# Performance work log

Measured on AMD Instinct MI355X. Metric: run time of the kernel, lower is better.

Reference implementation:

```python
import jax, jax.numpy as jnp
import numpy as np

H = 512; EMB = 300; TAGE = 20; TRE = 20
VOCAB = 50000; NTAGS = 50; NTRANS = 100; NCONST = 80
B = 128; S = 256; T = 512; R = S // 2


def _lstm_scan(x, Wih, Whh, b):
    # x: [N, L, D] -> hidden states [N, L, H]; torch gate order i, f, g, o
    N = x.shape[0]; Hh = Whh.shape[1]
    xg = jnp.einsum('nld,gd->nlg', x, Wih) + b  # precompute input projections
    def step(carry, xg_t):
        h, c = carry
        g = xg_t + h @ Whh.T
        i, f, gg, o = jnp.split(g, 4, axis=-1)
        c = jax.nn.sigmoid(f) * c + jax.nn.sigmoid(i) * jnp.tanh(gg)
        h = jax.nn.sigmoid(o) * jnp.tanh(c)
        return (h, c), h
    h0 = jnp.zeros((N, Hh), x.dtype)
    _, hs = jax.lax.scan(step, (h0, h0), jnp.swapaxes(xg, 0, 1))
    return jnp.swapaxes(hs, 0, 1)


def setup_inputs() -> dict:
    key = jax.random.key(0)
    ks = iter(jax.random.split(key, 40))
    def p(shape, scale):
        return jax.random.normal(next(ks), shape, jnp.float32) * jnp.float32(scale)
    def lstm_p(din):
        s = 1.0 / np.sqrt(H)
        return p((4 * H, din), s), p((4 * H, H), s), p((4 * H,), s)
    inp = {}
    inp['word_idx'] = jax.random.randint(next(ks), (B, S), 0, VOCAB)
    inp['tag_idx'] = jax.random.randint(next(ks), (B, S), 0, NTAGS)
    inp['transition_idx'] = jax.random.randint(next(ks), (B, T), 0, NTRANS)
    inp['label_idx'] = jax.random.randint(next(ks), (B, R), 0, NCONST)
    inp['emb'] = p((VOCAB, EMB), 1.0)
    inp['tag_emb'] = p((NTAGS, TAGE), 1.0)
    inp['tr_emb'] = p((NTRANS, TRE), 1.0)
    inp['const_emb'] = p((NCONST, H), 1.0)
    inp['word_Wih'], inp['word_Whh'], inp['word_b'] = lstm_p(EMB + TAGE)
    inp['tr_Wih'], inp['tr_Whh'], inp['tr_b'] = lstm_p(TRE)
    inp['con_Wih'], inp['con_Whh'], inp['con_b'] = lstm_p(H)
    inp['fwd_Wih'], inp['fwd_Whh'], inp['fwd_b'] = lstm_p(H)
    inp['bwd_Wih'], inp['bwd_Whh'], inp['bwd_b'] = lstm_p(H)
    inp['w2c_W'] = p((H, H), 1.0 / np.sqrt(H)); inp['w2c_b'] = jnp.zeros((H,), jnp.float32)
    inp['red_W'] = p((H, 2 * H), 1.0 / np.sqrt(2 * H)); inp['red_b'] = jnp.zeros((H,), jnp.float32)
    inp['out_W'] = p((NTRANS, 3 * H), 1.0 / np.sqrt(3 * H)); inp['out_b'] = jnp.zeros((NTRANS,), jnp.float32)
    return inp


def reference(word_idx, tag_idx, transition_idx, label_idx, emb, tag_emb, tr_emb, const_emb, word_Wih, word_Whh, word_b, tr_Wih, tr_Whh, tr_b, con_Wih, con_Whh, con_b, fwd_Wih, fwd_Whh, fwd_b, bwd_Wih, bwd_Whh, bwd_b, w2c_W, w2c_b, red_W, red_b, out_W, out_b):
    Bn, Sn = word_idx.shape
    Rn = label_idx.shape[1]
    # initial_word_queue: word emb + tag emb -> word LSTM
    word_in = jnp.concatenate([emb[word_idx], tag_emb[tag_idx]], axis=-1)  # [B,S,EMB+TAGE]
    word_h = _lstm_scan(word_in, word_Wih, word_Whh, word_b)              # [B,S,H]
    # transform_word_to_constituent
    c0 = word_h @ w2c_W.T + w2c_b                                         # [B,S,H]
    # build_constituent: label emb + 2 children through fwd/bwd reduce LSTMs
    lab = const_emb[label_idx]                                            # [B,R,H]
    ch0 = c0[:, 0::2][:, :Rn]; ch1 = c0[:, 1::2][:, :Rn]
    fwd_seq = jnp.stack([lab, ch0, ch1], axis=2).reshape(Bn * Rn, 3, -1)
    bwd_seq = jnp.stack([lab, ch1, ch0], axis=2).reshape(Bn * Rn, 3, -1)
    fh = _lstm_scan(fwd_seq, fwd_Wih, fwd_Whh, fwd_b)[:, -1]
    bh = _lstm_scan(bwd_seq, bwd_Wih, bwd_Whh, bwd_b)[:, -1]
    red = jnp.tanh(jnp.concatenate([fh, bh], -1) @ red_W.T + red_b).reshape(Bn, Rn, -1)
    # push_constituent: constituent LSTMCell scan over built constituents
    const_h = _lstm_scan(red, con_Wih, con_Whh, con_b)[:, -1]             # [B,H]
    # push_transition: transition LSTMCell scan
    tr_h = _lstm_scan(tr_emb[transition_idx], tr_Wih, tr_Whh, tr_b)[:, -1]  # [B,H]
    # forward(): W over concat(word_hx, transition_hx, constituent_hx)
    hx = jnp.concatenate([word_h[:, -1], tr_h, const_h], axis=-1)         # [B,3H]
    return hx @ out_W.T + out_b                                           # [B,NTRANS]
```

## Files before the change

### kernel.cpp

```cpp
#include <hip/hip_runtime.h>

typedef unsigned short u16;
typedef unsigned int u32;
typedef unsigned long long u64;
typedef __attribute__((ext_vector_type(8))) short short8;
typedef __attribute__((ext_vector_type(4))) float f32x4;

namespace {
constexpr int kS  = 256;
constexpr int kT  = 512;
constexpr int kNT = 100;
constexpr int LDST = 40;
}

__device__ __forceinline__ float bf(u16 v){ return __uint_as_float(((u32)v)<<16); }
__device__ __forceinline__ u16 f2bf(float f){
  u32 u = __float_as_uint(f);
  return (u16)((u + 0x7fffu + ((u>>16)&1u)) >> 16);
}
__device__ __forceinline__ float sigm(float x){ return 1.f/(1.f+__expf(-x)); }
__device__ __forceinline__ float tanha(float x){ return 2.f/(1.f+__expf(-2.f*x)) - 1.f; }
__device__ __forceinline__ float wred(float v){
  #pragma unroll
  for (int off=32; off>0; off>>=1) v += __shfl_xor(v, off, 64);
  return v;
}

__device__ __forceinline__ void st_sys_u32(void* p, u32 v){
  __hip_atomic_store((u32*)p, v, __ATOMIC_RELAXED, __HIP_MEMORY_SCOPE_SYSTEM);
}
__device__ __forceinline__ u32 ld_sys_u32(const void* p){
  return __hip_atomic_load((const u32*)p, __ATOMIC_RELAXED, __HIP_MEMORY_SCOPE_SYSTEM);
}

__global__ void k_zero(u32* p, int n){
  const int i = blockIdx.x*256 + threadIdx.x;
  if (i < n) p[i] = 0;
}

struct SeqJob {
  u16* hseq;
  const u16* xg; const int* idx;
  float* c_io;
  const u16* Bw;
  u32* flags;
  int s_begin, s_end, mode, c_store;
};

__global__ __launch_bounds__(256,1) void k_seq2(SeqJob jA, SeqJob jB)
{
  __shared__ u16 Bs[32*520];
  __shared__ float c_lds[128*9];
  __shared__ float sc[4*4*16*20];
  const SeqJob j = (blockIdx.x < 64) ? jA : jB;
  const int gb = blockIdx.x & 63;
  const int tid = threadIdx.x;
  const int ln = tid & 63, w = tid >> 6, wm = w * 32;
  const int fr = ln & 15, koff = (ln >> 4) * 8;
  const int n0 = gb * 32, jh0 = gb * 8;

  for (int e = tid; e < 2048; e += 256) {
    const int cl = e >> 6, kb = (e & 63) * 8;
    *(uint4*)&Bs[cl*520 + kb] = *(const uint4*)&j.Bw[(size_t)(n0+cl)*512 + kb];
  }
  for (int e = tid; e < 1024; e += 256) {
    const int m = e >> 3, jj = e & 7;
    c_lds[m*9 + jj] = j.c_io[(size_t)m*512 + jh0 + jj];
  }
  __syncthreads();

  const size_t aoff0 = (size_t)(wm + fr)*512 + koff;
  const size_t aoff1 = (size_t)(wm + 16 + fr)*512 + koff;
  const int cr = (ln>>4)*4, cc = ln&15;
  const int trow = ln>>2, pp = ln&3, ntp = pp>>1, cp = pp&1;
  const f32x4 z4 = {0.f,0.f,0.f,0.f};

  for (int s = j.s_begin; s < j.s_end; ++s) {
    const u16* Ab = j.hseq + (size_t)((s-1)&255)*65536;
    u16* hout     = j.hseq + (size_t)(s&255)*65536;
    const u16* xgs = (j.mode == 0) ? (j.xg + (size_t)s*262144) : j.xg;

    int xrow[2];
    #pragma unroll
    for (int mt = 0; mt < 2; ++mt) {
      const int m = wm + mt*16 + trow;
      if (j.mode == 1)      xrow[mt] = j.idx[(size_t)m*512 + s];
      else if (j.mode == 0) xrow[mt] = m;
      else                  xrow[mt] = m*128 + s;
    }

    uint4 aq0[16], aq1[16];
    #pragma unroll
    for (int kt = 0; kt < 16; ++kt) {
      aq0[kt] = *(const uint4*)&Ab[aoff0 + kt*32];
      aq1[kt] = *(const uint4*)&Ab[aoff1 + kt*32];
    }
    uint4 xqv[2];
    #pragma unroll
    for (int mt = 0; mt < 2; ++mt)
      xqv[mt] = *(const uint4*)&xgs[(size_t)xrow[mt]*2048 + n0 + ntp*16 + cp*8];

    f32x4 acc[2][2] = {{z4,z4},{z4,z4}};
    #pragma unroll
    for (int kt = 0; kt < 16; ++kt) {
      union { uint4 q; short8 v; } ua, ub;
      ua.q = aq0[kt]; ub.q = aq1[kt];
      const short8 b0 = *(const short8*)&Bs[fr*520 + kt*32 + koff];
      const short8 b1 = *(const short8*)&Bs[(16+fr)*520 + kt*32 + koff];
      acc[0][0] = __builtin_amdgcn_mfma_f32_16x16x32_bf16(ua.v, b0, acc[0][0], 0,0,0);
      acc[0][1] = __builtin_amdgcn_mfma_f32_16x16x32_bf16(ua.v, b1, acc[0][1], 0,0,0);
      acc[1][0] = __builtin_amdgcn_mfma_f32_16x16x32_bf16(ub.v, b0, acc[1][0], 0,0,0);
      acc[1][1] = __builtin_amdgcn_mfma_f32_16x16x32_bf16(ub.v, b1, acc[1][1], 0,0,0);
    }

    #pragma unroll
    for (int mt=0; mt<2; ++mt)
      #pragma unroll
      for (int nt=0; nt<2; ++nt) {
        float* scb = &sc[(size_t)(w*4 + mt*2 + nt)*320];
        #pragma unroll
        for (int ri=0; ri<4; ++ri) scb[(cr+ri)*20 + cc] = acc[mt][nt][ri];
      }
    #pragma unroll
    for (int mt=0; mt<2; ++mt) {
      const int m = wm + mt*16 + trow;
      const float* scb = &sc[(size_t)(w*4+mt*2+ntp)*320 + trow*20 + cp*8];
      const float4 zlo = *(const float4*)&scb[0];
      const float4 zhi = *(const float4*)&scb[4];
      union { uint4 u4; u16 h[8]; } xq;
      xq.u4 = xqv[mt];
      const int cj = m*9 + ntp*4 + cp*2;
      float h0, h1;
      {
        const float i_ = sigm(zlo.x + bf(xq.h[0]));
        const float f_ = sigm(zlo.y + bf(xq.h[1]));
        const float g_ = tanha(zlo.z + bf(xq.h[2]));
        const float o_ = sigm(zlo.w + bf(xq.h[3]));
        const float cn = f_*c_lds[cj] + i_*g_;
        c_lds[cj] = cn;
        h0 = o_*tanha(cn);
      }
      {
        const float i_ = sigm(zhi.x + bf(xq.h[4]));
        const float f_ = sigm(zhi.y + bf(xq.h[5]));
        const float g_ = tanha(zhi.z + bf(xq.h[6]));
        const float o_ = sigm(zhi.w + bf(xq.h[7]));
        const float cn = f_*c_lds[cj+1] + i_*g_;
        c_lds[cj+1] = cn;
        h1 = o_*tanha(cn);
      }
      const u32 pk = (u32)f2bf(h0) | ((u32)f2bf(h1) << 16);
      st_sys_u32(&hout[(size_t)m*512 + jh0 + ntp*4 + cp*2], pk);
    }

    __builtin_amdgcn_s_waitcnt(0);
    __syncthreads();
    if (tid == 0)
      st_sys_u32(j.flags + gb, (u32)s);
    if (s + 1 < j.s_end) {
      if (tid < 64) {
        while (true) {
          u32 f = ld_sys_u32(j.flags + tid);
          if (__all((int)(f >= (u32)s))) break;
          __builtin_amdgcn_s_sleep(1);
        }
      }
      __syncthreads();
    }
  }
  if (j.c_store) {
    __syncthreads();
    for (int e = tid; e < 1024; e += 256) {
      const int m = e >> 3, jj = e & 7;
      j.c_io[(size_t)m*512 + jh0 + jj] = c_lds[m*9 + jj];
    }
  }
}

__device__ __forceinline__ void gemm_core(
    const u16* __restrict__ A, const u16* __restrict__ B, int K,
    int m0, int n0, u16* As, u16* Bs, f32x4 acc[4][4], int tid)
{
  const int lane = tid & 63;
  const int w = tid >> 6;
  const int wm = (w & 1) * 64, wn = (w >> 1) * 64;
  const int fr = lane & 15;
  const int fq = (lane >> 4) * 8;
  for (int k0 = 0; k0 < K; k0 += 32) {
    __syncthreads();
    #pragma unroll
    for (int it = 0; it < 2; ++it) {
      const int l = tid + it * 256;
      const int r = l >> 2, kq = (l & 3) * 8;
      *(uint4*)&As[r * LDST + kq] = *(const uint4*)&A[(size_t)(m0 + r) * K + k0 + kq];
      *(uint4*)&Bs[r * LDST + kq] = *(const uint4*)&B[(size_t)(n0 + r) * K + k0 + kq];
    }
    __syncthreads();
    short8 af[4], bfr[4];
    #pragma unroll
    for (int t = 0; t < 4; ++t) {
      af[t]  = *(const short8*)&As[(wm + t * 16 + fr) * LDST + fq];
      bfr[t] = *(const short8*)&Bs[(wn + t * 16 + fr) * LDST + fq];
    }
    #pragma unroll
    for (int mt = 0; mt < 4; ++mt)
      #pragma unroll
      for (int nt = 0; nt < 4; ++nt)
        acc[mt][nt] = __builtin_amdgcn_mfma_f32_16x16x32_bf16(af[mt], bfr[nt], acc[mt][nt], 0, 0, 0);
  }
}

__global__ __launch_bounds__(256) void k_gemm(
    const u16* __restrict__ A, const u16* __restrict__ B, u16* __restrict__ C,
    const float* __restrict__ bias, int K, int N, int tanh_flag)
{
  __shared__ u16 As[128 * LDST];
  __shared__ u16 Bs[128 * LDST];
  const int tid = threadIdx.x;
  const int m0 = blockIdx.x * 128, n0 = blockIdx.y * 128;
  f32x4 acc[4][4];
  const f32x4 z4 = {0.f, 0.f, 0.f, 0.f};
  #pragma unroll
  for (int mt = 0; mt < 4; ++mt)
    #pragma unroll
    for (int nt = 0; nt < 4; ++nt) acc[mt][nt] = z4;

  gemm_core(A, B, K, m0, n0, As, Bs, acc, tid);

  const int lane = tid & 63;
  const int w = tid >> 6;
  const int wm = (w & 1) * 64, wn = (w >> 1) * 64;
  const int cr = (lane >> 4) * 4, cc = lane & 15;
  #pragma unroll
  for (int mt = 0; mt < 4; ++mt)
    #pragma unroll
    for (int nt = 0; nt < 4; ++nt)
      #pragma unroll
      for (int ri = 0; ri < 4; ++ri) {
        const int row = m0 + wm + mt * 16 + cr + ri;
        const int col = n0 + wn + nt * 16 + cc;
        float v = acc[mt][nt][ri];
        if (bias) v += bias[col];
        if (tanh_flag) v = tanha(v);
        C[(size_t)row * N + col] = f2bf(v);
      }
}

__global__ __launch_bounds__(256) void k_lstm_cat(
    const u16* __restrict__ H, const u16* __restrict__ X,
    const u16* __restrict__ B, const float* __restrict__ bias,
    const int* __restrict__ idx, int cmode, int p0, int first,
    float* __restrict__ c_st, u16* __restrict__ h_out, int h_stride, int h_coloff)
{
  __shared__ u16 As[128 * LDST];
  __shared__ u16 Bs[128 * LDST];
  __shared__ float zb[64 * 128];
  const int tid = threadIdx.x;
  const int m0 = blockIdx.x * 128, n0 = blockIdx.y * 128;
  const int lane = tid & 63;
  const int w = tid >> 6;
  const int wm = (w & 1) * 64, wn = (w >> 1) * 64;
  const int fr = lane & 15, fq = (lane >> 4) * 8;
  f32x4 acc[4][4];
  const f32x4 z4 = {0.f, 0.f, 0.f, 0.f};
  #pragma unroll
  for (int mt = 0; mt < 4; ++mt)
    #pragma unroll
    for (int nt = 0; nt < 4; ++nt) acc[mt][nt] = z4;

  for (int k0 = first ? 512 : 0; k0 < 1024; k0 += 32) {
    __syncthreads();
    #pragma unroll
    for (int it = 0; it < 2; ++it) {
      const int l = tid + it * 256;
      const int r = l >> 2, kq = (l & 3) * 8;
      const int m = m0 + r;
      const u16* src;
      if (k0 < 512) {
        src = H + (size_t)m * 512 + k0 + kq;
      } else {
        long xr;
        if (cmode == 1)      xr = (long)(2 * (m & 127) + p0) * 128 + (m >> 7);
        else if (cmode == 2) xr = (long)idx[m];
        else                 xr = (long)m * 128 + p0;
        src = X + (size_t)xr * 512 + (k0 - 512) + kq;
      }
      *(uint4*)&As[r * LDST + kq] = *(const uint4*)src;
      *(uint4*)&Bs[r * LDST + kq] = *(const uint4*)&B[(size_t)(n0 + r) * 1024 + k0 + kq];
    }
    __syncthreads();
    short8 af[4], bfr[4];
    #pragma unroll
    for (int t = 0; t < 4; ++t) {
      af[t]  = *(const short8*)&As[(wm + t * 16 + fr) * LDST + fq];
      bfr[t] = *(const short8*)&Bs[(wn + t * 16 + fr) * LDST + fq];
    }
    #pragma unroll
    for (int mt = 0; mt < 4; ++mt)
      #pragma unroll
      for (int nt = 0; nt < 4; ++nt)
        acc[mt][nt] = __builtin_amdgcn_mfma_f32_16x16x32_bf16(af[mt], bfr[nt], acc[mt][nt], 0, 0, 0);
  }

  const int cr = (lane >> 4) * 4, cc = lane & 15;
  #pragma unroll
  for (int half = 0; half < 2; ++half) {
    __syncthreads();
    if (wm == half * 64) {
      #pragma unroll
      for (int mt = 0; mt < 4; ++mt)
        #pragma unroll
        for (int nt = 0; nt < 4; ++nt)
          #pragma unroll
          for (int ri = 0; ri < 4; ++ri)
            zb[(mt * 16 + cr + ri) * 128 + wn + nt * 16 + cc] = acc[mt][nt][ri];
    }
    __syncthreads();
    for (int c = tid; c < 2048; c += 256) {
      const int rl = c >> 5;
      const int q  = c & 31;
      const int m  = m0 + half * 64 + rl;
      const int jh = (n0 >> 2) + q;
      const float4 bv = *(const float4*)&bias[n0 + q * 4];
      const float4 zv = *(const float4*)&zb[rl * 128 + q * 4];
      const float i_ = sigm(zv.x + bv.x);
      const float f_ = sigm(zv.y + bv.y);
      const float g_ = tanha(zv.z + bv.z);
      const float o_ = sigm(zv.w + bv.w);
      const size_t ci = (size_t)m * 512 + jh;
      const float cold = first ? 0.f : c_st[ci];
      const float cn = f_ * cold + i_ * g_;
      c_st[ci] = cn;
      h_out[(size_t)m * h_stride + h_coloff + jh] = f2bf(o_ * tanha(cn));
    }
  }
}

__global__ __launch_bounds__(256) void k_gate0(
    const u16* __restrict__ xg, int xg_mode, int p0,
    const int* __restrict__ idx, int istride,
    float* __restrict__ c_st, u16* __restrict__ h_out, int h_stride, int h_coloff, int M)
{
  const int id = blockIdx.x * 256 + threadIdx.x;
  if (id >= M * 512) return;
  const int m = id >> 9, jh = id & 511;
  long xr;
  if (xg_mode == 0) xr = (long)m * p0;
  else              xr = (long)idx[(size_t)m * istride];
  const ushort4 xq = *(const ushort4*)&xg[(size_t)xr * 2048 + jh * 4];
  const float i_ = sigm(bf(xq.x));
  const float g_ = tanha(bf(xq.z));
  const float o_ = sigm(bf(xq.w));
  const float cn = i_ * g_;
  c_st[(size_t)m * 512 + jh] = cn;
  h_out[(size_t)m * h_stride + h_coloff + jh] = f2bf(o_ * tanha(cn));
}

__global__ void k_perm_w(const float* __restrict__ in, u16* __restrict__ out,
                         int Ksrc, int Kfill, int Ktot, int coff)
{
  const int rp = blockIdx.x;
  const int g = rp & 3, jh = rp >> 2;
  const float* src = in + (size_t)(g * 512 + jh) * Ksrc;
  for (int k = threadIdx.x; k < Kfill; k += 256)
    out[(size_t)rp * Ktot + coff + k] = f2bf(k < Ksrc ? src[k] : 0.f);
}
__global__ void k_perm_b(const float* __restrict__ in, float* __restrict__ out)
{
  const int rp = blockIdx.x * 256 + threadIdx.x;
  out[rp] = in[(rp & 3) * 512 + (rp >> 2)];
}
__global__ void k_cvt(const float* __restrict__ in, u16* __restrict__ out, int n)
{
  const int i = blockIdx.x * 256 + threadIdx.x;
  if (i < n) out[i] = f2bf(in[i]);
}
__global__ void k_pad2d(const float* __restrict__ in, u16* __restrict__ out,
                        int Rin, int Kin, int Kout)
{
  const int r = blockIdx.x;
  for (int k = threadIdx.x; k < Kout; k += 256)
    out[(size_t)r * Kout + k] = f2bf((r < Rin && k < Kin) ? in[(size_t)r * Kin + k] : 0.f);
}
__global__ void k_gather_word(const int* __restrict__ widx, const int* __restrict__ tidx,
                              const float* __restrict__ emb, const float* __restrict__ temb,
                              u16* __restrict__ Aw)
{
  const int row = blockIdx.x;
  const int s = row >> 7, b = row & 127;
  const int wi = widx[b * kS + s];
  const int ti = tidx[b * kS + s];
  for (int t = threadIdx.x; t < 320; t += 256)
    Aw[(size_t)row * 320 + t] = f2bf(t < 300 ? emb[(size_t)wi * 300 + t] : temb[ti * 20 + t - 300]);
}

__global__ __launch_bounds__(256) void k_out(
    const u16* __restrict__ wh, const u16* __restrict__ trh, const u16* __restrict__ conh,
    const float* __restrict__ W, const float* __restrict__ bias, float* __restrict__ out)
{
  const int wid = blockIdx.x * 4 + (threadIdx.x >> 6);
  const int lane = threadIdx.x & 63;
  const int b = wid / kNT;
  const int t = wid - b * kNT;
  const u16* s0 = wh + (size_t)b * 512;
  const u16* s1 = trh + (size_t)b * 512;
  const u16* s2 = conh + (size_t)b * 512;
  const float* wr = W + (size_t)t * 1536;
  float acc = 0.f;
  #pragma unroll
  for (int i = 0; i < 8; ++i) acc += bf(s0[i * 64 + lane]) * wr[i * 64 + lane];
  #pragma unroll
  for (int i = 0; i < 8; ++i) acc += bf(s1[i * 64 + lane]) * wr[512 + i * 64 + lane];
  #pragma unroll
  for (int i = 0; i < 8; ++i) acc += bf(s2[i * 64 + lane]) * wr[1024 + i * 64 + lane];
  acc = wred(acc);
  if (lane == 0) out[(size_t)b * kNT + t] = acc + bias[t];
}

extern "C" void kernel_launch(void* const* d_in, const int* in_sizes, int n_in,
                              void* d_out, int out_size, void* d_ws, size_t ws_size,
                              hipStream_t stream)
{
  (void)in_sizes; (void)n_in; (void)out_size; (void)ws_size;
  const int* word_idx = (const int*)d_in[0];
  const int* tag_idx  = (const int*)d_in[1];
  const int* tr_idx   = (const int*)d_in[2];
  const int* lab_idx  = (const int*)d_in[3];
  const float* emb       = (const float*)d_in[4];
  const float* tag_emb   = (const float*)d_in[5];
  const float* tr_emb    = (const float*)d_in[6];
  const float* const_emb = (const float*)d_in[7];
  const float* word_Wih = (const float*)d_in[8];
  const float* word_Whh = (const float*)d_in[9];
  const float* word_b   = (const float*)d_in[10];
  const float* tr_Wih = (const float*)d_in[11];
  const float* tr_Whh = (const float*)d_in[12];
  const float* tr_b   = (const float*)d_in[13];
  const float* con_Wih = (const float*)d_in[14];
  const float* con_Whh = (const float*)d_in[15];
  const float* con_b   = (const float*)d_in[16];
  const float* fwd_Wih = (const float*)d_in[17];
  const float* fwd_Whh = (const float*)d_in[18];
  const float* fwd_b   = (const float*)d_in[19];
  const float* bwd_Wih = (const float*)d_in[20];
  const float* bwd_Whh = (const float*)d_in[21];
  const float* bwd_b   = (const float*)d_in[22];
  const float* w2c_W = (const float*)d_in[23];
  const float* w2c_b = (const float*)d_in[24];
  const float* red_W = (const float*)d_in[25];
  const float* red_b = (const float*)d_in[26];
  const float* out_W = (const float*)d_in[27];
  const float* out_b = (const float*)d_in[28];

  char* p = (char*)d_ws;
  auto alloc = [&](size_t bytes)->void* {
    void* r = (void*)p; p += (bytes + 255) & ~(size_t)255; return r;
  };
  u16* word_h = (u16*)alloc((size_t)33554432);
  char* R     = (char*)alloc((size_t)167772160);
  u16* A_word = (u16*)(R);
  u16* XGword = (u16*)(R + 33554432);
  u16* trseq  = (u16*)(R);
  u16* c0     = (u16*)(R + 33554432);
  u16* h1     = (u16*)(R + 67108864);
  u16* h2     = (u16*)(R + 83886080);
  float* c_big= (float*)(R + 100663296);
  u16* fb     = (u16*)(R + 134217728);
  u16* red    = (u16*)(R);
  u16* XG_con = (u16*)(R + 67108864);
  u16* conseq = (u16*)(R + 134217728);
  u16* wWih = (u16*)alloc((size_t)2048*320*2);
  u16* wWhh = (u16*)alloc((size_t)2048*512*2);
  u16* tWih = (u16*)alloc((size_t)2048*32*2);
  u16* tWhh = (u16*)alloc((size_t)2048*512*2);
  u16* cWihp = (u16*)alloc((size_t)2048*512*2);
  u16* cWhhp = (u16*)alloc((size_t)2048*512*2);
  u16* fWcat = (u16*)alloc((size_t)2048*1024*2);
  u16* bWcat = (u16*)alloc((size_t)2048*1024*2);
  u16* fWih  = (u16*)alloc((size_t)2048*512*2);
  u16* bWih  = (u16*)alloc((size_t)2048*512*2);
  u16* w2cWb = (u16*)alloc((size_t)512*512*2);
  u16* redWb = (u16*)alloc((size_t)512*1024*2);
  u16* A80   = (u16*)alloc((size_t)128*512*2);
  u16* Atr   = (u16*)alloc((size_t)128*32*2);
  u16* tbltr = (u16*)alloc((size_t)128*2048*2);
  u16* tbl0  = (u16*)alloc((size_t)128*2048*2);
  float* b_word = (float*)alloc(2048*4);
  float* b_tr   = (float*)alloc(2048*4);
  float* b_con  = (float*)alloc(2048*4);
  float* b_fwd  = (float*)alloc(2048*4);
  float* b_bwd  = (float*)alloc(2048*4);
  float* c_word = (float*)alloc((size_t)128*512*4);
  float* c_tr   = (float*)alloc((size_t)128*512*4);
  float* c_con  = (float*)alloc((size_t)128*512*4);
  u32* flags = (u32*)alloc((size_t)4*64*4);

  k_zero<<<1,256,0,stream>>>(flags, 4*64);

  k_perm_w<<<2048,256,0,stream>>>(word_Wih, wWih, 320, 320, 320, 0);
  k_perm_w<<<2048,256,0,stream>>>(word_Whh, wWhh, 512, 512, 512, 0);
  k_perm_w<<<2048,256,0,stream>>>(tr_Wih,   tWih, 20,  32,  32,  0);
  k_perm_w<<<2048,256,0,stream>>>(tr_Whh,   tWhh, 512, 512, 512, 0);
  k_perm_w<<<2048,256,0,stream>>>(con_Wih,  cWihp, 512, 512, 512, 0);
  k_perm_w<<<2048,256,0,stream>>>(con_Whh,  cWhhp, 512, 512, 512, 0);
  k_perm_w<<<2048,256,0,stream>>>(fwd_Whh,  fWcat, 512, 512, 1024, 0);
  k_perm_w<<<2048,256,0,stream>>>(fwd_Wih,  fWcat, 512, 512, 1024, 512);
  k_perm_w<<<2048,256,0,stream>>>(bwd_Whh,  bWcat, 512, 512, 1024, 0);
  k_perm_w<<<2048,256,0,stream>>>(bwd_Wih,  bWcat, 512, 512, 1024, 512);
  k_perm_w<<<2048,256,0,stream>>>(fwd_Wih,  fWih, 512, 512, 512, 0);
  k_perm_w<<<2048,256,0,stream>>>(bwd_Wih,  bWih, 512, 512, 512, 0);
  k_perm_b<<<8,256,0,stream>>>(word_b, b_word);
  k_perm_b<<<8,256,0,stream>>>(tr_b,   b_tr);
  k_perm_b<<<8,256,0,stream>>>(con_b,  b_con);
  k_perm_b<<<8,256,0,stream>>>(fwd_b,  b_fwd);
  k_perm_b<<<8,256,0,stream>>>(bwd_b,  b_bwd);
  k_cvt<<<1024,256,0,stream>>>(w2c_W, w2cWb, 512*512);
  k_cvt<<<2048,256,0,stream>>>(red_W, redWb, 512*1024);
  k_pad2d<<<128,256,0,stream>>>(const_emb, A80, 80, 512, 512);
  k_pad2d<<<128,256,0,stream>>>(tr_emb,    Atr, 100, 20, 32);
  k_gather_word<<<32768,256,0,stream>>>(word_idx, tag_idx, emb, tag_emb, A_word);

  k_gemm<<<dim3(256,16),256,0,stream>>>(A_word, wWih, XGword, b_word, 320, 2048, 0);
  k_gemm<<<dim3(1,16),256,0,stream>>>(Atr, tWih, tbltr, b_tr, 32, 2048, 0);

  k_gate0<<<256,256,0,stream>>>(XGword, 0, 1, nullptr, 0, c_word, word_h, 512, 0, 128);
  k_gate0<<<256,256,0,stream>>>(tbltr, 2, 0, tr_idx, 512, c_tr, trseq, 512, 0, 128);

  SeqJob jw { word_h, XGword, nullptr, c_word, wWhh, flags + 0*64, 1, 256, 0, 0 };
  SeqJob jt1{ trseq,  tbltr,  tr_idx,  c_tr,   tWhh, flags + 1*64, 1, 256, 1, 1 };
  k_seq2<<<128,256,0,stream>>>(jw, jt1);

  k_gemm<<<dim3(256,4),256,0,stream>>>(word_h, w2cWb, c0, w2c_b, 512, 512, 0);

  k_gemm<<<dim3(1,16),256,0,stream>>>(A80, fWih, tbl0, b_fwd, 512, 2048, 0);
  k_gate0<<<32768,256,0,stream>>>(tbl0, 2, 0, lab_idx, 1, c_big, h1, 512, 0, 16384);
  k_lstm_cat<<<dim3(128,16),256,0,stream>>>(h1, c0, fWcat, b_fwd, nullptr, 1, 0, 0, c_big, h2, 512, 0);
  k_lstm_cat<<<dim3(128,16),256,0,stream>>>(h2, c0, fWcat, b_fwd, nullptr, 1, 1, 0, c_big, fb, 1024, 0);
  k_gemm<<<dim3(1,16),256,0,stream>>>(A80, bWih, tbl0, b_bwd, 512, 2048, 0);
  k_gate0<<<32768,256,0,stream>>>(tbl0, 2, 0, lab_idx, 1, c_big, h1, 512, 0, 16384);
  k_lstm_cat<<<dim3(128,16),256,0,stream>>>(h1, c0, bWcat, b_bwd, nullptr, 1, 1, 0, c_big, h2, 512, 0);
  k_lstm_cat<<<dim3(128,16),256,0,stream>>>(h2, c0, bWcat, b_bwd, nullptr, 1, 0, 0, c_big, fb, 1024, 512);

  k_gemm<<<dim3(128,4),256,0,stream>>>(fb, redWb, red, red_b, 1024, 512, 1);

  k_gemm<<<dim3(128,16),256,0,stream>>>(red, cWihp, XG_con, b_con, 512, 2048, 0);

  k_gate0<<<256,256,0,stream>>>(XG_con, 0, 128, nullptr, 0, c_con, conseq, 512, 0, 128);

  SeqJob jc { conseq, XG_con, nullptr, c_con, cWhhp, flags + 2*64, 1,   128, 2, 0 };
  SeqJob jt2{ trseq,  tbltr,  tr_idx,  c_tr,  tWhh,  flags + 3*64, 256, 512, 1, 0 };
  k_seq2<<<128,256,0,stream>>>(jc, jt2);

  k_out<<<3200,256,0,stream>>>(word_h + (size_t)255*65536, trseq + (size_t)255*65536,
                               conseq + (size_t)127*65536, out_W, out_b, (float*)d_out);
}
```

Before: 5.241 ms.

## Replace per-step flag barrier with poison-value polling on hidden-state buffers

The per-step cross-block flag barrier in the persistent LSTM recurrence kernel is removed. Hidden-state buffers are pre-filled with a poison pattern, and each block spins re-loading its A operand with cache-bypassing loads until no poison word remains. The transition sequence now uses a full 512-slot buffer instead of a 256-slot ring, so poisoned slots are never reused. The next step's input-gate loads and indices are prefetched early. This removes the __syncthreads, flag store and all-block poll each step, at the cost of extra fill kernels, more memory traffic and a reliance on dword-granular store visibility and on bf16 pairs never equalling the poison pattern.

```diff
diff --git a/kernel.cpp b/kernel.cpp
--- a/kernel.cpp
+++ b/kernel.cpp
@@ -5,12 +5,14 @@
 typedef unsigned long long u64;
 typedef __attribute__((ext_vector_type(8))) short short8;
 typedef __attribute__((ext_vector_type(4))) float f32x4;
+typedef __attribute__((ext_vector_type(4))) unsigned int u32x4;
 
 namespace {
 constexpr int kS  = 256;
 constexpr int kT  = 512;
 constexpr int kNT = 100;
 constexpr int LDST = 40;
+constexpr u32 POISON = 0xFFFFFFFFu;
 }
 
 __device__ __forceinline__ float bf(u16 v){ return __uint_as_float(((u32)v)<<16); }
@@ -25,17 +27,23 @@
   for (int off=32; off>0; off>>=1) v += __shfl_xor(v, off, 64);
   return v;
 }
-
-__device__ __forceinline__ void st_sys_u32(void* p, u32 v){
-  __hip_atomic_store((u32*)p, v, __ATOMIC_RELAXED, __HIP_MEMORY_SCOPE_SYSTEM);
-}
-__device__ __forceinline__ u32 ld_sys_u32(const void* p){
-  return __hip_atomic_load((const u32*)p, __ATOMIC_RELAXED, __HIP_MEMORY_SCOPE_SYSTEM);
-}
-
-__global__ void k_zero(u32* p, int n){
+__device__ __forceinline__ short8 as_s8(u32x4 x){ union{u32x4 q; short8 v;} u; u.q=x; return u.v; }
+__device__ __forceinline__ u32 chk4(u32x4 v){
+  return (u32)((v.x==POISON)|(v.y==POISON)|(v.z==POISON)|(v.w==POISON));
+}
+
+#define LDX(d, b, o) asm volatile("global_load_dwordx4 %0, %1, off offset:" o : "=v"(d) : "v"(b))
+#define LDP(d, b, o) asm volatile("global_load_dwordx4 %0, %1, off offset:" o " sc0 sc1" : "=v"(d) : "v"(b))
+#define LDI(d, b)    asm volatile("global_load_dword %0, %1, off" : "=v"(d) : "v"(b))
+#define STW(p, v)    asm volatile("global_store_dword %0, %1, off sc0 sc1" :: "v"(p), "v"(v) : "memory")
+#define WAITV0       do{ asm volatile("s_waitcnt vmcnt(0)" ::: "memory"); __builtin_amdgcn_sched_barrier(0); }while(0)
+
+__global__ void k_fill(u32* __restrict__ p, int n4){
   const int i = blockIdx.x*256 + threadIdx.x;
-  if (i < n) p[i] = 0;
+  if (i < n4) {
+    u32x4 v = {POISON, POISON, POISON, POISON};
+    *(u32x4*)&p[(size_t)i*4] = v;
+  }
 }
 
 struct SeqJob {
@@ -43,8 +51,7 @@
   const u16* xg; const int* idx;
   float* c_io;
   const u16* Bw;
-  u32* flags;
-  int s_begin, s_end, mode, c_store;
+  int s_begin, s_end, mode, smask, c_store;
 };
 
 __global__ __launch_bounds__(256,1) void k_seq2(SeqJob jA, SeqJob jB)
@@ -60,8 +67,8 @@
   const int n0 = gb * 32, jh0 = gb * 8;
 
   for (int e = tid; e < 2048; e += 256) {
-    const int cl = e >> 6, kb = (e & 63) * 8;
-    *(uint4*)&Bs[cl*520 + kb] = *(const uint4*)&j.Bw[(size_t)(n0+cl)*512 + kb];
+    const int cl_ = e >> 6, kb = (e & 63) * 8;
+    *(u32x4*)&Bs[cl_*520 + kb] = *(const u32x4*)&j.Bw[(size_t)(n0+cl_)*512 + kb];
   }
   for (int e = tid; e < 1024; e += 256) {
     const int m = e >> 3, jj = e & 7;
@@ -74,43 +81,74 @@
   const int cr = (ln>>4)*4, cc = ln&15;
   const int trow = ln>>2, pp = ln&3, ntp = pp>>1, cp = pp&1;
   const f32x4 z4 = {0.f,0.f,0.f,0.f};
+  const int mA = wm + trow;
+  const int mB = wm + 16 + trow;
+  const int xgcol = n0 + ntp*16 + cp*8;
+
+  u32x4 xqA, xqB;
+  {
+    long ivA = mA, ivB = mB;
+    if (j.mode == 1) {
+      ivA = j.idx[(size_t)mA*512 + j.s_begin];
+      ivB = j.idx[(size_t)mB*512 + j.s_begin];
+    } else if (j.mode == 2) {
+      ivA = (long)mA*128 + j.s_begin;
+      ivB = (long)mB*128 + j.s_begin;
+    }
+    const u16* xgs0 = (j.mode == 0) ? (j.xg + (size_t)j.s_begin*262144) : j.xg;
+    const u16* pA = &xgs0[(size_t)ivA*2048 + xgcol];
+    const u16* pB = &xgs0[(size_t)ivB*2048 + xgcol];
+    LDX(xqA, pA, "0");
+    LDX(xqB, pB, "0");
+  }
+  int inA = 0, inB = 0;
+
+#define PISS(kt, o) LDP(aq0[kt], pa0, o); LDP(aq1[kt], pa1, o)
+#define ISSUE_ALL \
+  PISS(0,"0");    PISS(1,"64");   PISS(2,"128");  PISS(3,"192"); \
+  PISS(4,"256");  PISS(5,"320");  PISS(6,"384");  PISS(7,"448"); \
+  PISS(8,"512");  PISS(9,"576");  PISS(10,"640"); PISS(11,"704"); \
+  PISS(12,"768"); PISS(13,"832"); PISS(14,"896"); PISS(15,"960")
+#define CHECK_ALL(bad) \
+  { bad = 0; _Pragma("unroll") \
+    for (int kt = 0; kt < 16; ++kt) bad |= chk4(aq0[kt]) | chk4(aq1[kt]); }
 
   for (int s = j.s_begin; s < j.s_end; ++s) {
-    const u16* Ab = j.hseq + (size_t)((s-1)&255)*65536;
-    u16* hout     = j.hseq + (size_t)(s&255)*65536;
-    const u16* xgs = (j.mode == 0) ? (j.xg + (size_t)s*262144) : j.xg;
-
-    int xrow[2];
-    #pragma unroll
-    for (int mt = 0; mt < 2; ++mt) {
-      const int m = wm + mt*16 + trow;
-      if (j.mode == 1)      xrow[mt] = j.idx[(size_t)m*512 + s];
-      else if (j.mode == 0) xrow[mt] = m;
-      else                  xrow[mt] = m*128 + s;
-    }
-
-    uint4 aq0[16], aq1[16];
+    const u16* Ab = j.hseq + (size_t)((s-1) & j.smask)*65536;
+    u16* hout     = j.hseq + (size_t)(s & j.smask)*65536;
+    const u16* pa0 = Ab + aoff0;
+    const u16* pa1 = Ab + aoff1;
+    const bool more = (s + 1 < j.s_end);
+
+    if (j.mode == 1 && more) {
+      const int* ia = &j.idx[(size_t)mA*512 + s + 1];
+      const int* ib = &j.idx[(size_t)mB*512 + s + 1];
+      LDI(inA, ia);
+      LDI(inB, ib);
+    }
+
+    u32x4 aq0[16], aq1[16];
+    ISSUE_ALL;
+    WAITV0;
+    u32 bad; CHECK_ALL(bad);
+    while (bad) {
+      __builtin_amdgcn_s_sleep(1);
+      ISSUE_ALL;
+      WAITV0;
+      CHECK_ALL(bad);
+    }
+
+    f32x4 acc[2][2] = {{z4,z4},{z4,z4}};
     #pragma unroll
     for (int kt = 0; kt < 16; ++kt) {
-      aq0[kt] = *(const uint4*)&Ab[aoff0 + kt*32];
-      aq1[kt] = *(const uint4*)&Ab[aoff1 + kt*32];
-    }
-    uint4 xqv[2];
-    #pragma unroll
-    for (int mt = 0; mt < 2; ++mt)
-      xqv[mt] = *(const uint4*)&xgs[(size_t)xrow[mt]*2048 + n0 + ntp*16 + cp*8];
-
-    f32x4 acc[2][2] = {{z4,z4},{z4,z4}};
-    #pragma unroll
-    for (int kt = 0; kt < 16; ++kt) {
-      union { uint4 q; short8 v; } ua, ub;
-      ua.q = aq0[kt]; ub.q = aq1[kt];
       const short8 b0 = *(const short8*)&Bs[fr*520 + kt*32 + koff];
       const short8 b1 = *(const short8*)&Bs[(16+fr)*520 + kt*32 + koff];
-      acc[0][0] = __builtin_amdgcn_mfma_f32_16x16x32_bf16(ua.v, b0, acc[0][0], 0,0,0);
-      acc[0][1] = __builtin_amdgcn_mfma_f32_16x16x32_bf16(ua.v, b1, acc[0][1], 0,0,0);
-      acc[1][0] = __builtin_amdgcn_mfma_f32_16x16x32_bf16(ub.v, b0, acc[1][0], 0,0,0);
-      acc[1][1] = __builtin_amdgcn_mfma_f32_16x16x32_bf16(ub.v, b1, acc[1][1], 0,0,0);
+      const short8 a0v = as_s8(aq0[kt]);
+      const short8 a1v = as_s8(aq1[kt]);
+      acc[0][0] = __builtin_amdgcn_mfma_f32_16x16x32_bf16(a0v, b0, acc[0][0], 0,0,0);
+      acc[0][1] = __builtin_amdgcn_mfma_f32_16x16x32_bf16(a0v, b1, acc[0][1], 0,0,0);
+      acc[1][0] = __builtin_amdgcn_mfma_f32_16x16x32_bf16(a1v, b0, acc[1][0], 0,0,0);
+      acc[1][1] = __builtin_amdgcn_mfma_f32_16x16x32_bf16(a1v, b1, acc[1][1], 0,0,0);
     }
 
     #pragma unroll
@@ -123,12 +161,12 @@
       }
     #pragma unroll
     for (int mt=0; mt<2; ++mt) {
-      const int m = wm + mt*16 + trow;
+      const int m = mt ? mB : mA;
       const float* scb = &sc[(size_t)(w*4+mt*2+ntp)*320 + trow*20 + cp*8];
       const float4 zlo = *(const float4*)&scb[0];
       const float4 zhi = *(const float4*)&scb[4];
-      union { uint4 u4; u16 h[8]; } xq;
-      xq.u4 = xqv[mt];
+      union { u32x4 u4; u16 h[8]; } xq;
+      xq.u4 = mt ? xqB : xqA;
       const int cj = m*9 + ntp*4 + cp*2;
       float h0, h1;
       {
@@ -150,22 +188,18 @@
         h1 = o_*tanha(cn);
       }
       const u32 pk = (u32)f2bf(h0) | ((u32)f2bf(h1) << 16);
-      st_sys_u32(&hout[(size_t)m*512 + jh0 + ntp*4 + cp*2], pk);
-    }
-
-    __builtin_amdgcn_s_waitcnt(0);
-    __syncthreads();
-    if (tid == 0)
-      st_sys_u32(j.flags + gb, (u32)s);
-    if (s + 1 < j.s_end) {
-      if (tid < 64) {
-        while (true) {
-          u32 f = ld_sys_u32(j.flags + tid);
-          if (__all((int)(f >= (u32)s))) break;
-          __builtin_amdgcn_s_sleep(1);
-        }
-      }
-      __syncthreads();
+      u32* hp = (u32*)&hout[(size_t)m*512 + jh0 + ntp*4 + cp*2];
+      STW(hp, pk);
+    }
+
+    if (more) {
+      const u16* xgs1 = (j.mode == 0) ? (j.xg + (size_t)(s+1)*262144) : j.xg;
+      long xrA = (j.mode == 0) ? (long)mA : (j.mode == 1 ? (long)inA : ((long)mA*128 + s + 1));
+      long xrB = (j.mode == 0) ? (long)mB : (j.mode == 1 ? (long)inB : ((long)mB*128 + s + 1));
+      const u16* pA = &xgs1[(size_t)xrA*2048 + xgcol];
+      const u16* pB = &xgs1[(size_t)xrB*2048 + xgcol];
+      LDX(xqA, pA, "0");
+      LDX(xqB, pB, "0");
     }
   }
   if (j.c_store) {
@@ -175,6 +209,9 @@
       j.c_io[(size_t)m*512 + jh0 + jj] = c_lds[m*9 + jj];
     }
   }
+#undef PISS
+#undef ISSUE_ALL
+#undef CHECK_ALL
 }
 
 __device__ __forceinline__ void gemm_core(
@@ -493,9 +530,6 @@
   float* c_word = (float*)alloc((size_t)128*512*4);
   float* c_tr   = (float*)alloc((size_t)128*512*4);
   float* c_con  = (float*)alloc((size_t)128*512*4);
-  u32* flags = (u32*)alloc((size_t)4*64*4);
-
-  k_zero<<<1,256,0,stream>>>(flags, 4*64);
 
   k_perm_w<<<2048,256,0,stream>>>(word_Wih, wWih, 320, 320, 320, 0);
   k_perm_w<<<2048,256,0,stream>>>(word_Whh, wWhh, 512, 512, 512, 0);
@@ -523,11 +557,14 @@
   k_gemm<<<dim3(256,16),256,0,stream>>>(A_word, wWih, XGword, b_word, 320, 2048, 0);
   k_gemm<<<dim3(1,16),256,0,stream>>>(Atr, tWih, tbltr, b_tr, 32, 2048, 0);
 
+  k_fill<<<8160,256,0,stream>>>((u32*)(word_h + 65536), 2088960);
+  k_fill<<<8160,256,0,stream>>>((u32*)(trseq + 65536), 2088960);
+
   k_gate0<<<256,256,0,stream>>>(XGword, 0, 1, nullptr, 0, c_word, word_h, 512, 0, 128);
   k_gate0<<<256,256,0,stream>>>(tbltr, 2, 0, tr_idx, 512, c_tr, trseq, 512, 0, 128);
 
-  SeqJob jw { word_h, XGword, nullptr, c_word, wWhh, flags + 0*64, 1, 256, 0, 0 };
-  SeqJob jt1{ trseq,  tbltr,  tr_idx,  c_tr,   tWhh, flags + 1*64, 1, 256, 1, 1 };
+  SeqJob jw { word_h, XGword, nullptr, c_word, wWhh, 1, 256, 0, 255, 0 };
+  SeqJob jt1{ trseq,  tbltr,  tr_idx,  c_tr,   tWhh, 1, 256, 1, 511, 1 };
   k_seq2<<<128,256,0,stream>>>(jw, jt1);
 
   k_gemm<<<dim3(256,4),256,0,stream>>>(word_h, w2cWb, c0, w2c_b, 512, 512, 0);
@@ -545,12 +582,15 @@
 
   k_gemm<<<dim3(128,16),256,0,stream>>>(red, cWihp, XG_con, b_con, 512, 2048, 0);
 
+  k_fill<<<8192,256,0,stream>>>((u32*)(trseq + (size_t)256*65536), 2097152);
+  k_fill<<<4064,256,0,stream>>>((u32*)(conseq + 65536), 1040384);
+
   k_gate0<<<256,256,0,stream>>>(XG_con, 0, 128, nullptr, 0, c_con, conseq, 512, 0, 128);
 
-  SeqJob jc { conseq, XG_con, nullptr, c_con, cWhhp, flags + 2*64, 1,   128, 2, 0 };
-  SeqJob jt2{ trseq,  tbltr,  tr_idx,  c_tr,  tWhh,  flags + 3*64, 256, 512, 1, 0 };
+  SeqJob jc { conseq, XG_con, nullptr, c_con, cWhhp, 1,   128, 2, 255, 0 };
+  SeqJob jt2{ trseq,  tbltr,  tr_idx,  c_tr,  tWhh,  256, 512, 1, 511, 0 };
   k_seq2<<<128,256,0,stream>>>(jc, jt2);
 
-  k_out<<<3200,256,0,stream>>>(word_h + (size_t)255*65536, trseq + (size_t)255*65536,
+  k_out<<<3200,256,0,stream>>>(word_h + (size_t)255*65536, trseq + (size_t)511*65536,
                                conseq + (size_t)127*65536, out_W, out_b, (float*)d_out);
 }
```

New measurement: 6.373 ms. 1.22x slower.
